# Optimization experiments

Hardware: AMD Instinct MI355X
Metric: run time of the kernel (lower is better)

The kernel has to match this reference:

```python
import jax, jax.numpy as jnp
import numpy as np

D = 256          # input_dim == layer_size
L = 2            # n_hidden_layers in ResLinear
B, S = 8, 4096
LR = 1e-3        # AdamW learning_rate
WD = 1e-2        # weight_decay
MAX_ALR = 0.1    # max adaptive lr
EPS = 1e-8       # AdamW eps


def _lmm(Ws, bs, x):
    # ResLinear: residual MLP blocks, hidden size D.
    # Ws: [L, D, D], bs: [L, D], x: [..., D]
    for i in range(L):
        x = x + jax.nn.silu(x @ Ws[i] + bs[i])
    return x


def setup_inputs() -> dict:
    key = jax.random.key(0)
    ks = jax.random.split(key, 9)
    scale = 0.05
    return {
        "x": jax.random.normal(ks[0], (B, S, D), dtype=jnp.float32),
        "Wk": jax.random.normal(ks[1], (D, D), dtype=jnp.float32) * scale,
        "Wq": jax.random.normal(ks[2], (D, D), dtype=jnp.float32) * scale,
        "Wv": jax.random.normal(ks[3], (D, D), dtype=jnp.float32) * scale,
        "Wlr": jax.random.normal(ks[4], (D, 1), dtype=jnp.float32) * scale,
        "blr": jnp.zeros((1,), dtype=jnp.float32),
        "Ws": jax.random.normal(ks[5], (L, D, D), dtype=jnp.float32) * scale,
        "bs": jnp.zeros((L, D), dtype=jnp.float32),
    }


def reference(x, Wk, Wq, Wv, Wlr, blr, Ws, bs):
    # Projections (LinearProjection: bias-free D->D linear)
    keys = x @ Wk          # [B, S, D]
    queries = x @ Wq       # [B, S, D]
    values = x @ Wv        # [B, S, D]
    # AdaptiveLR: sigmoid gate scaled to max_adaptive_lr, one scalar per token
    alr = (jax.nn.sigmoid(x @ Wlr + blr) * MAX_ALR).reshape(-1)  # [B*S]

    def loss_fn(params):
        Ws_, bs_ = params
        preds = _lmm(Ws_, bs_, keys).reshape(-1, D)
        tgt = values.reshape(-1, D)
        per_tok = jnp.mean((preds - tgt) ** 2, axis=-1)  # [B*S]
        return jnp.sum(per_tok * alr)

    gWs, gbs = jax.grad(loss_fn)((Ws, bs))

    # Single AdamW step from zero optimizer state (step=1):
    #   m_hat = g, v_hat = g^2  ->  p' = p*(1 - lr*wd) - lr * g / (|g| + eps)
    def adamw_step(p, g):
        return p * (1.0 - LR * WD) - LR * g / (jnp.sqrt(g * g) + EPS)

    nWs = adamw_step(Ws, gWs)
    nbs = adamw_step(bs, gbs)

    retrieved = _lmm(nWs, nbs, queries)  # [B, S, D]
    # surprises = -grads
    return retrieved, -gWs, -gbs
```

## Files before the change

kernel.cpp:

```cpp
#include <hip/hip_runtime.h>
#include <math.h>


#define NTOK 32768
#define NM ((size_t)NTOK * 256)
#define LRc 1e-3f
#define WDc 1e-2f
#define EPSc 1e-8f

typedef __attribute__((ext_vector_type(8))) short bf16x8;
typedef __attribute__((ext_vector_type(4))) float f32x4;

__device__ __forceinline__ float b2f(unsigned short u) {
    union { unsigned int i; float f; } c;
    c.i = ((unsigned int)u) << 16;
    return c.f;
}
__device__ __forceinline__ unsigned short f2b(float f) {
    union { float f; unsigned int i; } c;
    c.f = f;
    unsigned int i = c.i;
    return (unsigned short)((i + 0x7FFFu + ((i >> 16) & 1u)) >> 16);
}
__device__ __forceinline__ float sigm(float z) { return 1.f / (1.f + __expf(-z)); }
__device__ __forceinline__ float siluf(float z) { return z * sigm(z); }
__device__ __forceinline__ float dsiluf(float z) {
    float s = sigm(z);
    return s * (1.f + z * (1.f - s));
}
__device__ __forceinline__ void unpack4(uint2 u, float* f) {
    f[0] = b2f(u.x & 0xFFFF); f[1] = b2f(u.x >> 16);
    f[2] = b2f(u.y & 0xFFFF); f[3] = b2f(u.y >> 16);
}
__device__ __forceinline__ uint2 pack4(const float* f) {
    uint2 o;
    o.x = (unsigned)f2b(f[0]) | ((unsigned)f2b(f[1]) << 16);
    o.y = (unsigned)f2b(f[2]) | ((unsigned)f2b(f[3]) << 16);
    return o;
}

#define WSTR 264
#define SSTR 40

template <int EPI>
__global__ __launch_bounds__(512, 4) void wgemm_k(
    const unsigned short* __restrict__ A, const unsigned short* __restrict__ Bt,
    const float* __restrict__ bias, const unsigned short* __restrict__ Rin,
    const unsigned short* __restrict__ Zin, const unsigned short* __restrict__ Vb,
    const float* __restrict__ alr, unsigned short* __restrict__ Cb,
    float* __restrict__ Cf, unsigned short* __restrict__ Zout,
    unsigned short* __restrict__ Rout, size_t zcs) {
    __shared__ unsigned short Ws[128 * WSTR];
    __shared__ unsigned short Sc[8][16 * SSTR];
    Bt += (size_t)blockIdx.z * 65536;
    Cb += (size_t)blockIdx.z * zcs;
    const int n0 = blockIdx.x * 128, m0 = blockIdx.y * 128;
    const int tid = threadIdx.x, lane = tid & 63, wv = tid >> 6;
    const int cc = lane & 15, q = lane >> 4;

    const int t0 = m0 + wv * 16;
    const unsigned short* xp = A + (size_t)(t0 + cc) * 256 + q * 8;
    bf16x8 xf[8];
#pragma unroll
    for (int c = 0; c < 8; c++) xf[c] = *(const bf16x8*)(xp + c * 32);

#pragma unroll
    for (int it = 0; it < 8; it++) {
        int i = it * 512 + tid;
        int row = i >> 5, g8 = i & 31;
        *(uint4*)&Ws[row * WSTR + g8 * 8] =
            *(const uint4*)(Bt + (size_t)(n0 + row) * 256 + g8 * 8);
    }
    __syncthreads();

    f32x4 acc[8];
#pragma unroll
    for (int t = 0; t < 8; t++) acc[t] = (f32x4){0.f, 0.f, 0.f, 0.f};

#pragma unroll
    for (int c = 0; c < 8; c++) {
#pragma unroll
        for (int nt = 0; nt < 8; nt++) {
            bf16x8 wf = *(const bf16x8*)&Ws[(nt * 16 + cc) * WSTR + c * 32 + q * 8];
            acc[nt] = __builtin_amdgcn_mfma_f32_16x16x32_bf16(wf, xf[c],
                                                              acc[nt], 0, 0, 0);
        }
    }

    const int tok = t0 + cc;
    float lalr = 0.f;
    if (EPI == 5) lalr = alr[tok] * (2.f / 256.f);
    unsigned short* sc = &Sc[wv][0];
    const int rtok = lane >> 2, roct = (lane & 3) * 8;

#pragma unroll
    for (int pr = 0; pr < 4; pr++) {
        float o2[2][4], z2[2][4];
#pragma unroll
        for (int h = 0; h < 2; h++) {
            const int nt = pr * 2 + h;
            const int gcol = n0 + nt * 16 + q * 4;
            const size_t off = (size_t)tok * 256 + gcol;
            f32x4 c = acc[nt];
            float v[4] = {c[0], c[1], c[2], c[3]};
            if (EPI == 0) {
#pragma unroll
                for (int r = 0; r < 4; r++) o2[h][r] = v[r];
            } else if (EPI == 1) {
                float bv[4], a[4];
                *(float4*)bv = *(const float4*)(bias + gcol);
                unpack4(*(const uint2*)(A + off), a);
#pragma unroll
                for (int r = 0; r < 4; r++) {
                    float z = v[r] + bv[r];
                    z2[h][r] = z;
                    o2[h][r] = a[r] + siluf(z);
                }
            } else if (EPI == 5) {
                float bv[4], a[4], vv[4];
                *(float4*)bv = *(const float4*)(bias + gcol);
                unpack4(*(const uint2*)(A + off), a);
                unpack4(*(const uint2*)(Vb + off), vv);
#pragma unroll
                for (int r = 0; r < 4; r++) {
                    float z = v[r] + bv[r];
                    float h2 = a[r] + siluf(z);
                    float dh = lalr * (h2 - vv[r]);
                    o2[h][r] = dh * dsiluf(z);
                    z2[h][r] = dh;
                }
            } else if (EPI == 2) {
                float ri[4], zi[4];
                unpack4(*(const uint2*)(Rin + off), ri);
                unpack4(*(const uint2*)(Zin + off), zi);
#pragma unroll
                for (int r = 0; r < 4; r++)
                    o2[h][r] = (v[r] + ri[r]) * dsiluf(zi[r]);
            } else {
                float bv[4], a[4];
                *(float4*)bv = *(const float4*)(bias + gcol);
                unpack4(*(const uint2*)(A + off), a);
#pragma unroll
                for (int r = 0; r < 4; r++) o2[h][r] = a[r] + siluf(v[r] + bv[r]);
            }
            if (EPI == 4) {
                *(float4*)(Cf + off) = *(float4*)o2[h];
            }
        }
        if (EPI == 4) continue;
#pragma unroll
        for (int h = 0; h < 2; h++)
            *(uint2*)&sc[cc * SSTR + h * 16 + q * 4] = pack4(o2[h]);
        uint4 pk = *(const uint4*)&sc[rtok * SSTR + roct];
        *(uint4*)(Cb + (size_t)(t0 + rtok) * 256 + n0 + pr * 32 + roct) = pk;
        if (EPI == 1 || EPI == 5) {
#pragma unroll
            for (int h = 0; h < 2; h++)
                *(uint2*)&sc[cc * SSTR + h * 16 + q * 4] = pack4(z2[h]);
            uint4 pk2 = *(const uint4*)&sc[rtok * SSTR + roct];
            unsigned short* P2 = (EPI == 1) ? Zout : Rout;
            *(uint4*)(P2 + (size_t)(t0 + rtok) * 256 + n0 + pr * 32 + roct) = pk2;
        }
    }
}

__global__ __launch_bounds__(512, 4) void rgemm_k(
    const unsigned short* __restrict__ Kb, const unsigned short* __restrict__ h1b,
    const unsigned short* __restrict__ dz0b,
    const unsigned short* __restrict__ dz1b, float* __restrict__ pbuf) {
    __shared__ unsigned short As[128 * 64];
    __shared__ unsigned short Bs2[128 * 64];
    const int z = blockIdx.z, layer = z >> 6, zc = z & 63;
    const unsigned short* Ag = layer ? h1b : Kb;
    const unsigned short* Bg = layer ? dz1b : dz0b;
    const int t0 = zc * 512;
    const int j0 = blockIdx.x * 128, i0 = blockIdx.y * 128;
    const int tid = threadIdx.x, lane = tid & 63, wave = tid >> 6;

    const int half = tid >> 8;
    const int t9 = tid & 255;
    const int ptq = t9 >> 4;
    const int pi = (t9 & 15) * 8;
    const unsigned short* sg = half ? Bg : Ag;
    const int nb = half ? j0 : i0;
    unsigned int* dst = (unsigned int*)(half ? Bs2 : As);
    const unsigned short* gp = sg + (size_t)(t0 + ptq * 2) * 256 + nb + pi;

    const int wr = (wave >> 2) * 64, wc = (wave & 3) * 32;
    const int fr = lane & 15, fkb = lane >> 4;

    f32x4 acc[4][2];
#pragma unroll
    for (int i = 0; i < 4; i++)
#pragma unroll
        for (int j = 0; j < 2; j++) acc[i][j] = (f32x4){0.f, 0.f, 0.f, 0.f};

    uint4 u0 = *(const uint4*)gp;
    uint4 u1 = *(const uint4*)(gp + 256);
    gp += 32 * 256;

    for (int it = 0; it < 16; it++) {
        const unsigned int* w0 = (const unsigned int*)&u0;
        const unsigned int* w1 = (const unsigned int*)&u1;
#pragma unroll
        for (int ii = 0; ii < 8; ii++) {
            unsigned int lo = (w0[ii >> 1] >> (16 * (ii & 1))) & 0xFFFFu;
            unsigned int hi = (w1[ii >> 1] >> (16 * (ii & 1))) & 0xFFFFu;
            const int col = pi + ii;
            const int s2 = ((col >> 3) ^ col) & 3;
            const int s4 = ((col >> 2) ^ (col >> 5)) & 1;
            dst[col * 32 + (ptq ^ (s2 << 2) ^ (s4 << 4))] = lo | (hi << 16);
        }
        __syncthreads();
        if (it < 15) {
            u0 = *(const uint4*)gp;
            u1 = *(const uint4*)(gp + 256);
            gp += 32 * 256;
        }
        bf16x8 af[4], bfr[2];
#pragma unroll
        for (int i = 0; i < 4; i++) {
            const int col = wr + i * 16 + fr;
            const int s2 = ((col >> 3) ^ col) & 3;
            const int s4 = ((col >> 2) ^ (col >> 5)) & 1;
            af[i] = *(const bf16x8*)&As[col * 64 + (fkb ^ s2 ^ (s4 << 2)) * 8];
        }
#pragma unroll
        for (int j = 0; j < 2; j++) {
            const int col = wc + j * 16 + fr;
            const int s2 = ((col >> 3) ^ col) & 3;
            const int s4 = ((col >> 2) ^ (col >> 5)) & 1;
            bfr[j] = *(const bf16x8*)&Bs2[col * 64 + (fkb ^ s2 ^ (s4 << 2)) * 8];
        }
#pragma unroll
        for (int i = 0; i < 4; i++)
#pragma unroll
            for (int j = 0; j < 2; j++)
                acc[i][j] = __builtin_amdgcn_mfma_f32_16x16x32_bf16(
                    af[i], bfr[j], acc[i][j], 0, 0, 0);
        __syncthreads();
    }

    float* P = pbuf + (size_t)((layer << 6) + zc) * 65536;
    const int r0 = fkb * 4;
#pragma unroll
    for (int mi = 0; mi < 4; mi++)
#pragma unroll
        for (int ni = 0; ni < 2; ni++) {
            f32x4 c = acc[mi][ni];
#pragma unroll
            for (int r = 0; r < 4; r++)
                P[(size_t)(i0 + wr + mi * 16 + r0 + r) * 256 +
                  (j0 + wc + ni * 16 + fr)] = c[r];
        }
}

__global__ void reduce_k(const float* __restrict__ pbuf, float* __restrict__ accW) {
    int idx = blockIdx.x * 256 + threadIdx.x;
    int layer = idx >> 16, rc = idx & 65535;
    const float* p = pbuf + (size_t)layer * 64 * 65536 + rc;
    float s = 0.f;
#pragma unroll 8
    for (int c = 0; c < 64; c++) s += p[(size_t)c * 65536];
    accW[idx] = s;
}

__global__ __launch_bounds__(256) void colsum_k(const unsigned short* __restrict__ dz,
                                                float* __restrict__ gb) {
    const int col = threadIdx.x;
    const size_t r0 = (size_t)blockIdx.x * 128;
    float s0 = 0, s1 = 0, s2 = 0, s3 = 0;
    for (int r = 0; r < 128; r += 4) {
        s0 += b2f(dz[(r0 + r) * 256 + col]);
        s1 += b2f(dz[(r0 + r + 1) * 256 + col]);
        s2 += b2f(dz[(r0 + r + 2) * 256 + col]);
        s3 += b2f(dz[(r0 + r + 3) * 256 + col]);
    }
    atomicAdd(&gb[col], s0 + s1 + s2 + s3);
}

__global__ __launch_bounds__(256) void prep_k(const float* __restrict__ x,
                                              const float* __restrict__ Wlr,
                                              const float* __restrict__ blr,
                                              unsigned short* __restrict__ xb,
                                              float* __restrict__ alr) {
    const int wave = threadIdx.x >> 6, lane = threadIdx.x & 63;
    const int r = blockIdx.x * 4 + wave;
    float4 w = *(const float4*)(Wlr + lane * 4);
    float4 v = *(const float4*)(x + (size_t)r * 256 + lane * 4);
    float s = v.x * w.x + v.y * w.y + v.z * w.z + v.w * w.w;
    unsigned int p0 = (unsigned int)f2b(v.x) | ((unsigned int)f2b(v.y) << 16);
    unsigned int p1 = (unsigned int)f2b(v.z) | ((unsigned int)f2b(v.w) << 16);
    *(uint2*)(xb + (size_t)r * 256 + lane * 4) = make_uint2(p0, p1);
#pragma unroll
    for (int off = 32; off; off >>= 1) s += __shfl_down(s, off);
    if (lane == 0) alr[r] = 0.1f * sigm(s + blr[0]);
}

__global__ void wprep_k(const float* __restrict__ Wk, const float* __restrict__ Wq,
                        const float* __restrict__ Wv, const float* __restrict__ Ws,
                        unsigned short* __restrict__ wt) {
    const int z = blockIdx.y;
    const int idx = blockIdx.x * 256 + threadIdx.x;
    const float* src = z == 0 ? Wk : z == 1 ? Wq : z == 2 ? Wv
                     : z == 3 ? Ws : Ws + 65536;
    unsigned short* dst = wt + (size_t)z * 65536;
    float v = src[idx];
    if (z == 5)
        dst[idx] = f2b(v);
    else
        dst[(idx & 255) * 256 + (idx >> 8)] = f2b(v);
}

__global__ void adamw_w_k(const float* __restrict__ Ws,
                          const float* __restrict__ accW,
                          unsigned short* __restrict__ nWt,
                          float* __restrict__ outSW) {
    int idx = blockIdx.x * 256 + threadIdx.x;
    float g = accW[idx];
    outSW[idx] = -g;
    float nw = Ws[idx] * (1.f - LRc * WDc) - LRc * g / (fabsf(g) + EPSc);
    int l = idx >> 16, k = (idx >> 8) & 255, n = idx & 255;
    nWt[(size_t)l * 65536 + n * 256 + k] = f2b(nw);
}

__global__ void adamw_b_k(const float* __restrict__ bs,
                          const float* __restrict__ accB,
                          float* __restrict__ nb, float* __restrict__ outSb) {
    int idx = blockIdx.x * 256 + threadIdx.x;
    float g = accB[idx];
    outSb[idx] = -g;
    nb[idx] = bs[idx] * (1.f - LRc * WDc) - LRc * g / (fabsf(g) + EPSc);
}

__global__ void zero_k(float* p, int n) {
    int i = blockIdx.x * 256 + threadIdx.x;
    if (i < n) p[i] = 0.f;
}

extern "C" void kernel_launch(void* const* d_in, const int* in_sizes, int n_in,
                              void* d_out, int out_size, void* d_ws,
                              size_t ws_size, hipStream_t stream) {
    const float* x = (const float*)d_in[0];
    const float* Wk = (const float*)d_in[1];
    const float* Wq = (const float*)d_in[2];
    const float* Wv = (const float*)d_in[3];
    const float* Wlr = (const float*)d_in[4];
    const float* blr = (const float*)d_in[5];
    const float* Ws = (const float*)d_in[6];
    const float* bs = (const float*)d_in[7];

    unsigned short* S = (unsigned short*)d_ws;
    unsigned short* xb = S + 0 * NM;
    unsigned short* Kb = S + 1 * NM;
    unsigned short* Qb = S + 2 * NM;
    unsigned short* Vb = S + 3 * NM;
    unsigned short* z0b = S + 4 * NM;
    unsigned short* h1b = S + 5 * NM;
    unsigned short* dz1b = S + 6 * NM;
    unsigned short* dh2b = S + 7 * NM;
    unsigned short* dz0b = S + 8 * NM;
    float* pbuf = (float*)(S + 9 * NM);
    unsigned short* r1b = xb;

    unsigned short* wt = S + 11 * NM;
    unsigned short* W0t = wt + 3 * 65536;
    unsigned short* W1t = wt + 4 * 65536;
    unsigned short* W1b = wt + 5 * 65536;
    unsigned short* nW0t = wt + 6 * 65536;
    unsigned short* nW1t = wt + 7 * 65536;
    float* ft = (float*)(wt + 8 * 65536);
    float* alr = ft;
    float* accW = ft + 32768;
    float* accB = accW + 131072;
    float* nb = accB + 512;

    float* out_ret = (float*)d_out;
    float* out_sW = out_ret + NM;
    float* out_sb = out_sW + 131072;

    dim3 blk5(512);
    dim3 blk(256);
    dim3 g_tall(2, 256);

    zero_k<<<2, blk, 0, stream>>>(accB, 512);
    prep_k<<<8192, blk, 0, stream>>>(x, Wlr, blr, xb, alr);
    wprep_k<<<dim3(256, 6), blk, 0, stream>>>(Wk, Wq, Wv, Ws, wt);

    wgemm_k<0><<<dim3(2, 256, 3), blk5, 0, stream>>>(
        xb, wt, nullptr, nullptr, nullptr, nullptr, nullptr, Kb, nullptr,
        nullptr, nullptr, NM);

    wgemm_k<1><<<g_tall, blk5, 0, stream>>>(Kb, W0t, bs, nullptr, nullptr,
                                            nullptr, nullptr, h1b, nullptr,
                                            z0b, nullptr, 0);

    wgemm_k<5><<<g_tall, blk5, 0, stream>>>(h1b, W1t, bs + 256, nullptr,
                                            nullptr, Vb, alr, dz1b, nullptr,
                                            nullptr, dh2b, 0);
    colsum_k<<<256, blk, 0, stream>>>(dz1b, accB + 256);

    wgemm_k<2><<<g_tall, blk5, 0, stream>>>(dz1b, W1b, nullptr, dh2b, z0b,
                                            nullptr, nullptr, dz0b, nullptr,
                                            nullptr, nullptr, 0);
    colsum_k<<<256, blk, 0, stream>>>(dz0b, accB);

    rgemm_k<<<dim3(2, 2, 128), blk5, 0, stream>>>(Kb, h1b, dz0b, dz1b, pbuf);
    reduce_k<<<512, blk, 0, stream>>>(pbuf, accW);

    adamw_w_k<<<512, blk, 0, stream>>>(Ws, accW, nW0t, out_sW);
    adamw_b_k<<<2, blk, 0, stream>>>(bs, accB, nb, out_sb);

    wgemm_k<3><<<g_tall, blk5, 0, stream>>>(Qb, nW0t, nb, nullptr, nullptr,
                                            nullptr, nullptr, r1b, nullptr,
                                            nullptr, nullptr, 0);
    wgemm_k<4><<<g_tall, blk5, 0, stream>>>(r1b, nW1t, nb + 256, nullptr,
                                            nullptr, nullptr, nullptr, nullptr,
                                            out_ret, nullptr, nullptr, 0);
}
```

Before: 270.8 us.

## Fuse small kernels and halve split-K partitions in weight-gradient GEMM

Merges the input prep, weight conversion and bias-zeroing kernels into one launch. Merges the two bias column-sum kernels into one, and folds the split-K reduction into the AdamW update so the intermediate accumulated-gradient buffer is gone. The weight-gradient GEMM now uses 32 token chunks of 1024 instead of 64 chunks of 512, which halves the partial-sum traffic but also halves the number of blocks (256 instead of 512), lowering parallelism.

```diff
diff --git a/kernel.cpp b/kernel.cpp
--- a/kernel.cpp
+++ b/kernel.cpp
@@ -170,10 +170,10 @@
     const unsigned short* __restrict__ dz1b, float* __restrict__ pbuf) {
     __shared__ unsigned short As[128 * 64];
     __shared__ unsigned short Bs2[128 * 64];
-    const int z = blockIdx.z, layer = z >> 6, zc = z & 63;
+    const int z = blockIdx.z, layer = z >> 5, zc = z & 31;
     const unsigned short* Ag = layer ? h1b : Kb;
     const unsigned short* Bg = layer ? dz1b : dz0b;
-    const int t0 = zc * 512;
+    const int t0 = zc * 1024;
     const int j0 = blockIdx.x * 128, i0 = blockIdx.y * 128;
     const int tid = threadIdx.x, lane = tid & 63, wave = tid >> 6;
 
@@ -199,7 +199,7 @@
     uint4 u1 = *(const uint4*)(gp + 256);
     gp += 32 * 256;
 
-    for (int it = 0; it < 16; it++) {
+    for (int it = 0; it < 32; it++) {
         const unsigned int* w0 = (const unsigned int*)&u0;
         const unsigned int* w1 = (const unsigned int*)&u1;
 #pragma unroll
@@ -212,7 +212,7 @@
             dst[col * 32 + (ptq ^ (s2 << 2) ^ (s4 << 4))] = lo | (hi << 16);
         }
         __syncthreads();
-        if (it < 15) {
+        if (it < 31) {
             u0 = *(const uint4*)gp;
             u1 = *(const uint4*)(gp + 256);
             gp += 32 * 256;
@@ -241,7 +241,7 @@
         __syncthreads();
     }
 
-    float* P = pbuf + (size_t)((layer << 6) + zc) * 65536;
+    float* P = pbuf + (size_t)((layer << 5) + zc) * 65536;
     const int r0 = fkb * 4;
 #pragma unroll
     for (int mi = 0; mi < 4; mi++)
@@ -255,20 +255,40 @@
         }
 }
 
-__global__ void reduce_k(const float* __restrict__ pbuf, float* __restrict__ accW) {
-    int idx = blockIdx.x * 256 + threadIdx.x;
-    int layer = idx >> 16, rc = idx & 65535;
-    const float* p = pbuf + (size_t)layer * 64 * 65536 + rc;
-    float s = 0.f;
+__global__ __launch_bounds__(256) void gradstep_k(
+    const float* __restrict__ pbuf, const float* __restrict__ Ws,
+    const float* __restrict__ bs, const float* __restrict__ accB,
+    unsigned short* __restrict__ nWt, float* __restrict__ nb,
+    float* __restrict__ outSW, float* __restrict__ outSb) {
+    const int bi = blockIdx.x;
+    if (bi < 512) {
+        const int idx = bi * 256 + threadIdx.x;
+        const int layer = idx >> 16, rc = idx & 65535;
+        const float* p = pbuf + (size_t)layer * 32 * 65536 + rc;
+        float g = 0.f;
 #pragma unroll 8
-    for (int c = 0; c < 64; c++) s += p[(size_t)c * 65536];
-    accW[idx] = s;
-}
-
-__global__ __launch_bounds__(256) void colsum_k(const unsigned short* __restrict__ dz,
-                                                float* __restrict__ gb) {
+        for (int c = 0; c < 32; c++) g += p[(size_t)c * 65536];
+        outSW[idx] = -g;
+        float nw = Ws[idx] * (1.f - LRc * WDc) - LRc * g / (fabsf(g) + EPSc);
+        const int l = idx >> 16, k = (idx >> 8) & 255, n = idx & 255;
+        nWt[(size_t)l * 65536 + n * 256 + k] = f2b(nw);
+    } else {
+        for (int i = threadIdx.x; i < 512; i += 256) {
+            float g = accB[i];
+            outSb[i] = -g;
+            nb[i] = bs[i] * (1.f - LRc * WDc) - LRc * g / (fabsf(g) + EPSc);
+        }
+    }
+}
+
+__global__ __launch_bounds__(256) void colsum2_k(
+    const unsigned short* __restrict__ dz1, const unsigned short* __restrict__ dz0,
+    float* __restrict__ gb) {
+    const int bi = blockIdx.x;
+    const unsigned short* dz = (bi < 256) ? dz1 : dz0;
+    float* g = (bi < 256) ? gb + 256 : gb;
     const int col = threadIdx.x;
-    const size_t r0 = (size_t)blockIdx.x * 128;
+    const size_t r0 = (size_t)(bi & 255) * 128;
     float s0 = 0, s1 = 0, s2 = 0, s3 = 0;
     for (int r = 0; r < 128; r += 4) {
         s0 += b2f(dz[(r0 + r) * 256 + col]);
@@ -276,66 +296,45 @@
         s2 += b2f(dz[(r0 + r + 2) * 256 + col]);
         s3 += b2f(dz[(r0 + r + 3) * 256 + col]);
     }
-    atomicAdd(&gb[col], s0 + s1 + s2 + s3);
-}
-
-__global__ __launch_bounds__(256) void prep_k(const float* __restrict__ x,
-                                              const float* __restrict__ Wlr,
-                                              const float* __restrict__ blr,
-                                              unsigned short* __restrict__ xb,
-                                              float* __restrict__ alr) {
-    const int wave = threadIdx.x >> 6, lane = threadIdx.x & 63;
-    const int r = blockIdx.x * 4 + wave;
-    float4 w = *(const float4*)(Wlr + lane * 4);
-    float4 v = *(const float4*)(x + (size_t)r * 256 + lane * 4);
-    float s = v.x * w.x + v.y * w.y + v.z * w.z + v.w * w.w;
-    unsigned int p0 = (unsigned int)f2b(v.x) | ((unsigned int)f2b(v.y) << 16);
-    unsigned int p1 = (unsigned int)f2b(v.z) | ((unsigned int)f2b(v.w) << 16);
-    *(uint2*)(xb + (size_t)r * 256 + lane * 4) = make_uint2(p0, p1);
-#pragma unroll
-    for (int off = 32; off; off >>= 1) s += __shfl_down(s, off);
-    if (lane == 0) alr[r] = 0.1f * sigm(s + blr[0]);
-}
-
-__global__ void wprep_k(const float* __restrict__ Wk, const float* __restrict__ Wq,
-                        const float* __restrict__ Wv, const float* __restrict__ Ws,
-                        unsigned short* __restrict__ wt) {
-    const int z = blockIdx.y;
-    const int idx = blockIdx.x * 256 + threadIdx.x;
-    const float* src = z == 0 ? Wk : z == 1 ? Wq : z == 2 ? Wv
-                     : z == 3 ? Ws : Ws + 65536;
-    unsigned short* dst = wt + (size_t)z * 65536;
-    float v = src[idx];
-    if (z == 5)
-        dst[idx] = f2b(v);
-    else
-        dst[(idx & 255) * 256 + (idx >> 8)] = f2b(v);
-}
-
-__global__ void adamw_w_k(const float* __restrict__ Ws,
-                          const float* __restrict__ accW,
-                          unsigned short* __restrict__ nWt,
-                          float* __restrict__ outSW) {
-    int idx = blockIdx.x * 256 + threadIdx.x;
-    float g = accW[idx];
-    outSW[idx] = -g;
-    float nw = Ws[idx] * (1.f - LRc * WDc) - LRc * g / (fabsf(g) + EPSc);
-    int l = idx >> 16, k = (idx >> 8) & 255, n = idx & 255;
-    nWt[(size_t)l * 65536 + n * 256 + k] = f2b(nw);
-}
-
-__global__ void adamw_b_k(const float* __restrict__ bs,
-                          const float* __restrict__ accB,
-                          float* __restrict__ nb, float* __restrict__ outSb) {
-    int idx = blockIdx.x * 256 + threadIdx.x;
-    float g = accB[idx];
-    outSb[idx] = -g;
-    nb[idx] = bs[idx] * (1.f - LRc * WDc) - LRc * g / (fabsf(g) + EPSc);
-}
-
-__global__ void zero_k(float* p, int n) {
-    int i = blockIdx.x * 256 + threadIdx.x;
-    if (i < n) p[i] = 0.f;
+    atomicAdd(&g[col], s0 + s1 + s2 + s3);
+}
+
+__global__ __launch_bounds__(256) void prep_all_k(
+    const float* __restrict__ x, const float* __restrict__ Wlr,
+    const float* __restrict__ blr, const float* __restrict__ Wk,
+    const float* __restrict__ Wq, const float* __restrict__ Wv,
+    const float* __restrict__ Ws, unsigned short* __restrict__ xb,
+    float* __restrict__ alr, unsigned short* __restrict__ wt,
+    float* __restrict__ accB) {
+    const int bi = blockIdx.x;
+    if (bi < 8192) {
+        const int wave = threadIdx.x >> 6, lane = threadIdx.x & 63;
+        const int r = bi * 4 + wave;
+        float4 w = *(const float4*)(Wlr + lane * 4);
+        float4 v = *(const float4*)(x + (size_t)r * 256 + lane * 4);
+        float s = v.x * w.x + v.y * w.y + v.z * w.z + v.w * w.w;
+        unsigned int p0 = (unsigned int)f2b(v.x) | ((unsigned int)f2b(v.y) << 16);
+        unsigned int p1 = (unsigned int)f2b(v.z) | ((unsigned int)f2b(v.w) << 16);
+        *(uint2*)(xb + (size_t)r * 256 + lane * 4) = make_uint2(p0, p1);
+#pragma unroll
+        for (int off = 32; off; off >>= 1) s += __shfl_down(s, off);
+        if (lane == 0) alr[r] = 0.1f * sigm(s + blr[0]);
+    } else if (bi < 9728) {
+        const int b = bi - 8192;
+        const int z = b >> 8;
+        const int idx = (b & 255) * 256 + threadIdx.x;
+        const float* src = z == 0 ? Wk : z == 1 ? Wq : z == 2 ? Wv
+                         : z == 3 ? Ws : Ws + 65536;
+        unsigned short* dst = wt + (size_t)z * 65536;
+        float v = src[idx];
+        if (z == 5)
+            dst[idx] = f2b(v);
+        else
+            dst[(idx & 255) * 256 + (idx >> 8)] = f2b(v);
+    } else {
+        accB[threadIdx.x] = 0.f;
+        accB[threadIdx.x + 256] = 0.f;
+    }
 }
 
 extern "C" void kernel_launch(void* const* d_in, const int* in_sizes, int n_in,
@@ -371,8 +370,7 @@
     unsigned short* nW1t = wt + 7 * 65536;
     float* ft = (float*)(wt + 8 * 65536);
     float* alr = ft;
-    float* accW = ft + 32768;
-    float* accB = accW + 131072;
+    float* accB = ft + 32768;
     float* nb = accB + 512;
 
     float* out_ret = (float*)d_out;
@@ -383,9 +381,8 @@
     dim3 blk(256);
     dim3 g_tall(2, 256);
 
-    zero_k<<<2, blk, 0, stream>>>(accB, 512);
-    prep_k<<<8192, blk, 0, stream>>>(x, Wlr, blr, xb, alr);
-    wprep_k<<<dim3(256, 6), blk, 0, stream>>>(Wk, Wq, Wv, Ws, wt);
+    prep_all_k<<<9729, blk, 0, stream>>>(x, Wlr, blr, Wk, Wq, Wv, Ws, xb, alr,
+                                         wt, accB);
 
     wgemm_k<0><<<dim3(2, 256, 3), blk5, 0, stream>>>(
         xb, wt, nullptr, nullptr, nullptr, nullptr, nullptr, Kb, nullptr,
@@ -398,18 +395,17 @@
     wgemm_k<5><<<g_tall, blk5, 0, stream>>>(h1b, W1t, bs + 256, nullptr,
                                             nullptr, Vb, alr, dz1b, nullptr,
                                             nullptr, dh2b, 0);
-    colsum_k<<<256, blk, 0, stream>>>(dz1b, accB + 256);
 
     wgemm_k<2><<<g_tall, blk5, 0, stream>>>(dz1b, W1b, nullptr, dh2b, z0b,
                                             nullptr, nullptr, dz0b, nullptr,
                                             nullptr, nullptr, 0);
-    colsum_k<<<256, blk, 0, stream>>>(dz0b, accB);
-
-    rgemm_k<<<dim3(2, 2, 128), blk5, 0, stream>>>(Kb, h1b, dz0b, dz1b, pbuf);
-    reduce_k<<<512, blk, 0, stream>>>(pbuf, accW);
-
-    adamw_w_k<<<512, blk, 0, stream>>>(Ws, accW, nW0t, out_sW);
-    adamw_b_k<<<2, blk, 0, stream>>>(bs, accB, nb, out_sb);
+
+    colsum2_k<<<512, blk, 0, stream>>>(dz1b, dz0b, accB);
+
+    rgemm_k<<<dim3(2, 2, 64), blk5, 0, stream>>>(Kb, h1b, dz0b, dz1b, pbuf);
+
+    gradstep_k<<<513, blk, 0, stream>>>(pbuf, Ws, bs, accB, nW0t, nb, out_sW,
+                                        out_sb);
 
     wgemm_k<3><<<g_tall, blk5, 0, stream>>>(Qb, nW0t, nb, nullptr, nullptr,
                                             nullptr, nullptr, r1b, nullptr,
```

After: 252.4 us. 1.07x faster.
